# Kernel tuning notes

Measured on AMD Instinct MI355X. Metric: run time of the kernel, lower is better.

The kernel has to match this reference:

```python
import jax, jax.numpy as jnp
import numpy as np
from jax import lax

D_MODEL = 1024
D_INNER = 2 * D_MODEL  # expand=2
D_CONV = 4
BATCH = 4
SEQ = 4096


def setup_inputs() -> dict:
    key = jax.random.key(0)
    ks = jax.random.split(key, 10)
    s = 0.02
    return {
        "x": jax.random.normal(ks[0], (BATCH, SEQ, D_MODEL), jnp.float32),
        "in_proj_w": jax.random.normal(ks[1], (2 * D_INNER, D_MODEL), jnp.float32) * s,
        "in_proj_b": jnp.zeros((2 * D_INNER,), jnp.float32),
        "conv_w": jax.random.normal(ks[2], (D_INNER, 1, D_CONV), jnp.float32) * s,
        "conv_b": jnp.zeros((D_INNER,), jnp.float32),
        "dt_w": jax.random.normal(ks[3], (D_INNER, D_INNER), jnp.float32) * s,
        "dt_b": jnp.zeros((D_INNER,), jnp.float32),
        "b_w": jax.random.normal(ks[4], (D_INNER, D_INNER), jnp.float32) * s,
        "c_w": jax.random.normal(ks[5], (D_INNER, D_INNER), jnp.float32) * s,
        "A_log": jax.random.normal(ks[6], (D_INNER,), jnp.float32) * 0.02 - 2.0,
        "D_param": jnp.ones((D_INNER,), jnp.float32),
        "out_w": jax.random.normal(ks[7], (D_MODEL, D_INNER), jnp.float32) * s,
        "out_b": jnp.zeros((D_MODEL,), jnp.float32),
    }


def _mixer(x, in_proj_w, in_proj_b, conv_w, conv_b, dt_w, dt_b,
           b_w, c_w, A_log, D_param, out_w, out_b):
    B, L, _ = x.shape
    # input projection -> split into x/z branches
    xz = jnp.einsum("bld,ed->ble", x, in_proj_w) + in_proj_b
    x_branch, z_branch = jnp.split(xz, 2, axis=-1)  # each [B, L, d_inner]

    # causal depthwise conv1d (padding=d_conv-1 on the left == torch pad then [:L])
    u = jnp.transpose(x_branch, (0, 2, 1))  # [B, d_inner, L]
    u = lax.conv_general_dilated(
        u, conv_w,
        window_strides=(1,),
        padding=[(D_CONV - 1, 0)],
        dimension_numbers=("NCH", "OIH", "NCH"),
        feature_group_count=D_INNER,
    ) + conv_b[None, :, None]
    u = jnp.transpose(u, (0, 2, 1))  # [B, L, d_inner]
    u = jax.nn.silu(u)

    dt = jax.nn.softplus(jnp.einsum("bld,ed->ble", u, dt_w) + dt_b) + 1e-4
    B_t = jnp.tanh(jnp.einsum("bld,ed->ble", u, b_w))
    C_t = jnp.tanh(jnp.einsum("bld,ed->ble", u, c_w))

    A = jnp.exp(A_log)  # [d_inner]
    decay = jnp.exp(-dt * A)          # [B, L, d_inner]
    inc = (1.0 - decay) * B_t * u     # [B, L, d_inner]

    # linear recurrence: state_t = decay_t * state_{t-1} + inc_t
    def step(state, xs):
        d_t, i_t = xs
        state = d_t * state + i_t
        return state, state

    init = jnp.zeros((B, D_INNER), x.dtype)
    _, states = lax.scan(step, init,
                         (jnp.transpose(decay, (1, 0, 2)),
                          jnp.transpose(inc, (1, 0, 2))))  # [L, B, d_inner]
    states = jnp.transpose(states, (1, 0, 2))  # [B, L, d_inner]

    y = C_t * states + D_param * u
    y = y * jax.nn.sigmoid(z_branch)  # SiLU-style gate
    # dropout is identity in eval mode
    return jnp.einsum("ble,de->bld", y, out_w) + out_b


def reference(x, in_proj_w, in_proj_b, conv_w, conv_b, dt_w, dt_b,
              b_w, c_w, A_log, D_param, out_w, out_b):
    return _mixer(x, in_proj_w, in_proj_b, conv_w, conv_b, dt_w, dt_b,
                  b_w, c_w, A_log, D_param, out_w, out_b)
```

## Files before the change

### kernel.cpp

```cpp
#include <hip/hip_runtime.h>
#include <math.h>
#include <stdint.h>


#define BATCH 4
#define SEQ 4096
#define DMODEL 1024
#define DINNER 2048
#define CLS 32

typedef __bf16 bf16_t;
typedef __bf16 bf16x8 __attribute__((ext_vector_type(8)));
typedef float f32x4 __attribute__((ext_vector_type(4)));
typedef unsigned short ushort_t;
typedef unsigned short u16x4 __attribute__((ext_vector_type(4)));

enum { EP_F32 = 0, EP_BF = 1, EP_DBC = 2, EP_GATE = 3 };

__device__ __forceinline__ void gload_lds16(const void* g, void* l) {
    __builtin_amdgcn_global_load_lds(
        (const __attribute__((address_space(1))) void*)g,
        (__attribute__((address_space(3))) void*)l, 16, 0, 0);
}

__device__ __forceinline__ ushort_t f2bf(float f) {
    union { float f; uint32_t u; } c; c.f = f;
    uint32_t u = c.u;
    u += 0x7fffu + ((u >> 16) & 1u);
    return (ushort_t)(u >> 16);
}
__device__ __forceinline__ float bf2f(ushort_t h) {
    union { uint32_t u; float f; } c; c.u = (uint32_t)h << 16;
    return c.f;
}
__device__ __forceinline__ float tanh_exact(float v) {
    v = fminf(fmaxf(v, -15.f), 15.f);
    float e = __expf(2.f * v);
    return (e - 1.f) / (e + 1.f);
}
__device__ __forceinline__ float tanh_poly(float v) {
    float v2 = v * v;
    float t = v * (1.f - v2 * (0.33333333f - 0.13333333f * v2));
    if (__builtin_expect(fabsf(v) > 0.25f, 0)) t = tanh_exact(v);
    return t;
}
__device__ __forceinline__ float softplus_poly(float v) {
    float v2 = v * v;
    float s = 0.69314718f + 0.5f * v + v2 * (0.125f - 0.0052083333f * v2);
    if (__builtin_expect(fabsf(v) > 0.25f, 0))
        s = fmaxf(v, 0.f) + __logf(1.f + __expf(-fabsf(v)));
    return s;
}

#define WAITV2 asm volatile("s_waitcnt vmcnt(2)" ::: "memory")
#define WAITV0 asm volatile("s_waitcnt vmcnt(0)" ::: "memory")
#define WAITL0 asm volatile("s_waitcnt lgkmcnt(0)" ::: "memory")

__global__ __launch_bounds__(512) void gemm256_ep(
    const bf16_t* __restrict__ A, const bf16_t* __restrict__ W,
    const float* __restrict__ bias,
    ushort_t* __restrict__ T0, ushort_t* __restrict__ T1,
    ushort_t* __restrict__ T2, const float* __restrict__ alogp,
    int K, int Nout, int Lc, int a_bstride, int a_l0,
    int c_bstride, int c_l0, int mode)
{
    __shared__ __align__(16) char smem[131072];
    const int tid = threadIdx.x;
    const int lane = tid & 63;
    const int wid = tid >> 6;
    const int wm2 = wid >> 2;
    const int wn2 = wid & 3;
    const int wz = blockIdx.z;
    const bf16_t* Wmat = W + (size_t)wz * Nout * K;
    ushort_t* Tz = (wz == 0) ? T0 : (wz == 1 ? T1 : T2);
    const int n0 = blockIdx.x * 256;
    const int m0 = blockIdx.y * 256;
    const int bb = m0 / Lc;
    const int lb = m0 - bb * Lc;
    const bf16_t* Abase = A + ((size_t)bb * a_bstride + a_l0 + lb) * K;
    const bf16_t* Wbase = Wmat + (size_t)n0 * K;

    int r_[2], c_[2], lofs_[2];
#pragma unroll
    for (int i = 0; i < 2; ++i) {
        int ofs = tid * 16 + i * 8192;
        int r = ofs >> 7;
        int c16 = (ofs >> 4) & 7;
        r_[i] = r;
        c_[i] = (c16 ^ (r & 7)) << 3;
        lofs_[i] = ofs;
    }

    const int nt = K / 64;

    f32x4 acc[4][4][2];
#pragma unroll
    for (int q = 0; q < 4; ++q)
#pragma unroll
        for (int mi = 0; mi < 4; ++mi)
#pragma unroll
            for (int ni = 0; ni < 2; ++ni) acc[q][mi][ni] = f32x4{0.f, 0.f, 0.f, 0.f};

#pragma unroll
    for (int s = 0; s < 4; ++s) {
        const int isB_ = (s == 1 || s == 2);
        const int h_ = (s >= 2) ? 1 : 0;
        char* dst_ = smem + (isB_ ? 32768 : 0) + h_ * 16384;
        const bf16_t* g_ = isB_ ? Wbase : Abase;
        gload_lds16(g_ + (size_t)(h_ * 128 + r_[0]) * K + c_[0], dst_ + lofs_[0]);
        gload_lds16(g_ + (size_t)(h_ * 128 + r_[1]) * K + c_[1], dst_ + lofs_[1]);
    }

#define STAGE(S)                                                              \
    if (t + 1 < nt) {                                                         \
      char* base_ = smem + (((t + 1) & 1) ? 65536 : 0);                       \
      const int isB_ = ((S) == 1 || (S) == 2);                                \
      const int h_ = ((S) >= 2) ? 1 : 0;                                      \
      char* dst_ = base_ + (isB_ ? 32768 : 0) + h_ * 16384;                   \
      const bf16_t* g_ = isB_ ? Wbase : Abase;                                \
      const int k0_ = (t + 1) * 64;                                           \
      gload_lds16(g_ + (size_t)(h_ * 128 + r_[0]) * K + k0_ + c_[0],          \
                  dst_ + lofs_[0]);                                           \
      gload_lds16(g_ + (size_t)(h_ * 128 + r_[1]) * K + k0_ + c_[1],          \
                  dst_ + lofs_[1]);                                           \
    }

#define READ_A(dst, half)                                                     \
    _Pragma("unroll") for (int mi = 0; mi < 4; ++mi)                          \
    _Pragma("unroll") for (int ks = 0; ks < 2; ++ks) {                        \
      int row = (half) * 128 + wm2 * 64 + mi * 16 + (lane & 15);              \
      int cb = (ks * 64 + ((lane >> 4) << 4)) ^ ((row & 7) << 4);             \
      dst[mi][ks] = *(const bf16x8*)(bufb + row * 128 + cb);                  \
    }

#define READ_B(dst, half)                                                     \
    _Pragma("unroll") for (int ni = 0; ni < 2; ++ni)                          \
    _Pragma("unroll") for (int ks = 0; ks < 2; ++ks) {                        \
      int row = (half) * 128 + wn2 * 32 + ni * 16 + (lane & 15);              \
      int cb = (ks * 64 + ((lane >> 4) << 4)) ^ ((row & 7) << 4);             \
      dst[ni][ks] = *(const bf16x8*)(bufb + 32768 + row * 128 + cb);          \
    }

#define MMA(Q, AV, BV)                                                        \
    __builtin_amdgcn_s_setprio(1);                                            \
    _Pragma("unroll") for (int ks = 0; ks < 2; ++ks)                          \
    _Pragma("unroll") for (int mi = 0; mi < 4; ++mi)                          \
    _Pragma("unroll") for (int ni = 0; ni < 2; ++ni)                          \
      acc[(Q)][mi][ni] = __builtin_amdgcn_mfma_f32_16x16x32_bf16(             \
          AV[mi][ks], BV[ni][ks], acc[(Q)][mi][ni], 0, 0, 0);                 \
    __builtin_amdgcn_s_setprio(0);

    for (int t = 0; t < nt; ++t) {
        const char* bufb = smem + ((t & 1) ? 65536 : 0);
        bf16x8 av0[4][2], av1[4][2], bv0[2][2], bv1[2][2];
        STAGE(0)
        if (t + 1 < nt) { WAITV2; } else { WAITV0; }
        __builtin_amdgcn_s_barrier();
        READ_A(av0, 0)
        READ_B(bv0, 0)
        WAITL0; __builtin_amdgcn_sched_barrier(0);
        MMA(0, av0, bv0)
        STAGE(1)
        READ_B(bv1, 1)
        WAITL0; __builtin_amdgcn_sched_barrier(0);
        MMA(1, av0, bv1)
        STAGE(2)
        READ_A(av1, 1)
        WAITL0; __builtin_amdgcn_sched_barrier(0);
        MMA(3, av1, bv1)
        STAGE(3)
        MMA(2, av1, bv0)
        __builtin_amdgcn_s_barrier();
    }
#undef STAGE
#undef READ_A
#undef READ_B
#undef MMA

    __syncthreads();

    const size_t rowbase = (size_t)bb * c_bstride + c_l0 + lb;
    ushort_t* sm = (ushort_t*)smem;
#pragma unroll
    for (int q = 0; q < 4; ++q) {
#pragma unroll
        for (int ni = 0; ni < 2; ++ni) {
            const int col = (q & 1) * 128 + wn2 * 32 + ni * 16 + (lane & 15);
            float bv = 0.f, Ae = 0.f;
            if (mode == EP_BF || mode == EP_GATE) bv = bias[n0 + col];
            else if (mode == EP_DBC && wz == 0) {
                bv = bias[n0 + col]; Ae = __expf(alogp[n0 + col]);
            }
#pragma unroll
            for (int mi = 0; mi < 4; ++mi) {
#pragma unroll
                for (int r4 = 0; r4 < 4; ++r4) {
                    const int row = (q >> 1) * 128 + wm2 * 64 + mi * 16 +
                                    ((lane >> 4) << 2) + r4;
                    float v = acc[q][mi][ni][r4] + bv;
                    ushort_t o;
                    if (mode == EP_BF) {
                        o = f2bf(v);
                    } else if (mode == EP_GATE) {
                        const size_t off = (rowbase + row) * (size_t)Nout + n0 + col;
                        o = f2bf(bf2f(Tz[off]) / (1.f + __expf(-v)));
                    } else {
                        if (wz == 0)
                            o = f2bf(__expf(-(softplus_poly(v) + 1e-4f) * Ae));
                        else
                            o = f2bf(tanh_poly(v));
                    }
                    const int sbyte = row * 512 + (((col * 2) ^ ((row & 7) << 4)));
                    *(ushort_t*)((char*)sm + sbyte) = o;
                }
            }
        }
    }
    __syncthreads();
#pragma unroll
    for (int it = 0; it < 16; ++it) {
        const int b0 = tid * 16 + it * 8192;
        const int row = b0 >> 9;
        const int inrow = b0 & 511;
        const int src = row * 512 + (inrow ^ ((row & 7) << 4));
        int4 vv = *(const int4*)((const char*)sm + src);
        *(int4*)(Tz + (rowbase + row) * (size_t)Nout + n0 + (inrow >> 1)) = vv;
    }
}

#define GBK 64

__global__ __launch_bounds__(256) void gemm_f32out(
    const bf16_t* __restrict__ A, const bf16_t* __restrict__ W,
    const float* __restrict__ bias, float* __restrict__ Cf,
    int K, int Nout, int Lc, int a_bstride, int a_l0,
    int c_bstride, int c_l0)
{
    __shared__ __align__(16) bf16_t smem[128 * 128];
    bf16_t* sA = smem;
    bf16_t* sB = smem + 128 * GBK;
    const int tid = threadIdx.x;
    const int lane = tid & 63;
    const int wid = tid >> 6;
    const int wm = wid >> 1, wn = wid & 1;
    const int n0 = blockIdx.x * 128;
    const int m0 = blockIdx.y * 128;
    const int bb = m0 / Lc;
    const int lb = m0 - bb * Lc;
    const bf16_t* Abase = A + ((size_t)bb * a_bstride + a_l0 + lb) * K;
    const bf16_t* Wbase = W + (size_t)n0 * K;

    int st_row[4], st_sc[4], st_ofs[4];
#pragma unroll
    for (int i = 0; i < 4; ++i) {
        int ofs = tid * 16 + i * 4096;
        int r = ofs >> 7;
        int c16 = (ofs >> 4) & 7;
        st_ofs[i] = ofs;
        st_row[i] = r;
        st_sc[i] = (c16 ^ (r & 7)) << 3;
    }

    f32x4 acc[4][4];
#pragma unroll
    for (int i = 0; i < 4; ++i)
#pragma unroll
        for (int j = 0; j < 4; ++j) acc[i][j] = f32x4{0.f, 0.f, 0.f, 0.f};

    for (int k0 = 0; k0 < K; k0 += GBK) {
#pragma unroll
        for (int i = 0; i < 4; ++i) {
            gload_lds16(Abase + (size_t)st_row[i] * K + k0 + st_sc[i],
                        (char*)sA + st_ofs[i]);
            gload_lds16(Wbase + (size_t)st_row[i] * K + k0 + st_sc[i],
                        (char*)sB + st_ofs[i]);
        }
        __syncthreads();
#pragma unroll
        for (int ks = 0; ks < 2; ++ks) {
            bf16x8 av[4], bv[4];
#pragma unroll
            for (int mi = 0; mi < 4; ++mi) {
                int row = wm * 64 + mi * 16 + (lane & 15);
                int cb = (ks * 64 + ((lane >> 4) << 4)) ^ ((row & 7) << 4);
                av[mi] = *(const bf16x8*)((const char*)sA + row * 128 + cb);
            }
#pragma unroll
            for (int ni = 0; ni < 4; ++ni) {
                int row = wn * 64 + ni * 16 + (lane & 15);
                int cb = (ks * 64 + ((lane >> 4) << 4)) ^ ((row & 7) << 4);
                bv[ni] = *(const bf16x8*)((const char*)sB + row * 128 + cb);
            }
#pragma unroll
            for (int mi = 0; mi < 4; ++mi)
#pragma unroll
                for (int ni = 0; ni < 4; ++ni)
                    acc[mi][ni] = __builtin_amdgcn_mfma_f32_16x16x32_bf16(
                        av[mi], bv[ni], acc[mi][ni], 0, 0, 0);
        }
        __syncthreads();
    }

    const size_t rowbase = (size_t)bb * c_bstride + c_l0 + lb;
#pragma unroll
    for (int ni = 0; ni < 4; ++ni) {
        const int coll = wn * 64 + ni * 16 + (lane & 15);
        const float bv = bias ? bias[n0 + coll] : 0.f;
#pragma unroll
        for (int mi = 0; mi < 4; ++mi) {
#pragma unroll
            for (int r4 = 0; r4 < 4; ++r4) {
                const int rowl = wm * 64 + mi * 16 + ((lane >> 4) << 2) + r4;
                Cf[(rowbase + rowl) * (size_t)Nout + n0 + coll] =
                    acc[mi][ni][r4] + bv;
            }
        }
    }
}

__global__ __launch_bounds__(256) void cvt_bf16_k(
    const float4* __restrict__ in, ushort4* __restrict__ out, int n4)
{
    for (int i = blockIdx.x * 256 + threadIdx.x; i < n4; i += gridDim.x * 256) {
        float4 v = in[i];
        ushort4 o;
        o.x = f2bf(v.x); o.y = f2bf(v.y); o.z = f2bf(v.z); o.w = f2bf(v.w);
        out[i] = o;
    }
}

__global__ __launch_bounds__(256) void conv_silu_bf(
    const ushort_t* __restrict__ xb, const ushort_t* __restrict__ tailb,
    const float* __restrict__ cw, const float* __restrict__ cb,
    ushort_t* __restrict__ ubf, int Lc, int l0, size_t total)
{
    for (size_t idx = (size_t)blockIdx.x * 256 + threadIdx.x; idx < total;
         idx += (size_t)gridDim.x * 256) {
        int e = (int)(idx % DINNER);
        size_t r = idx / DINNER;
        int lp = (int)(r % Lc);
        int b  = (int)(r / Lc);
        float4 w = *(const float4*)(cw + (size_t)e * 4);
        float s = cb[e];
        const ushort_t* xbase = xb + (size_t)b * Lc * DINNER + e;
        if (lp >= 3) {
            s += bf2f(xbase[(size_t)(lp - 3) * DINNER]) * w.x
               + bf2f(xbase[(size_t)(lp - 2) * DINNER]) * w.y
               + bf2f(xbase[(size_t)(lp - 1) * DINNER]) * w.z
               + bf2f(xbase[(size_t)lp * DINNER]) * w.w;
        } else {
            const float ws4[4] = {w.x, w.y, w.z, w.w};
            const ushort_t* tbase = tailb + (size_t)b * 3 * DINNER + e;
#pragma unroll
            for (int j = 0; j < 4; ++j) {
                int ls = lp - 3 + j;
                float v;
                if (ls >= 0)            v = bf2f(xbase[(size_t)ls * DINNER]);
                else if (l0 + ls >= 0)  v = bf2f(tbase[(size_t)(3 + ls) * DINNER]);
                else                    v = 0.f;
                s += v * ws4[j];
            }
        }
        ubf[idx] = f2bf(s / (1.f + __expf(-s)));
    }
}

__global__ __launch_bounds__(256) void tail_update_bf(
    const ushort_t* __restrict__ xb, ushort_t* __restrict__ tailb, int Lc)
{
    int idx = blockIdx.x * 256 + threadIdx.x;
    if (idx >= BATCH * 3 * DINNER) return;
    int e = idx % DINNER;
    int j = (idx / DINNER) % 3;
    int b = idx / (3 * DINNER);
    tailb[idx] = xb[((size_t)b * Lc + Lc - 3 + j) * DINNER + e];
}

__global__ __launch_bounds__(256) void scan1_v4(
    const ushort_t* __restrict__ dec, const ushort_t* __restrict__ bt,
    const ushort_t* __restrict__ ub,
    float* __restrict__ P, float* __restrict__ S, int Lc, int nsub)
{
    int t = blockIdx.x * 256 + threadIdx.x;
    int e = (t & 511) << 2;
    int rest = t >> 9;
    int c = rest % nsub;
    int b = rest / nsub;
    size_t off = ((size_t)b * Lc + (size_t)c * CLS) * DINNER + e;
    float p[4] = {1.f, 1.f, 1.f, 1.f};
    float s[4] = {0.f, 0.f, 0.f, 0.f};
    for (int t0 = 0; t0 < CLS; ++t0) {
        size_t o = off + (size_t)t0 * DINNER;
        u16x4 d4 = *(const u16x4*)(dec + o);
        u16x4 b4 = *(const u16x4*)(bt + o);
        u16x4 u4 = *(const u16x4*)(ub + o);
#pragma unroll
        for (int j = 0; j < 4; ++j) {
            float d = bf2f(d4[j]);
            float inc = (1.f - d) * bf2f(b4[j]) * bf2f(u4[j]);
            s[j] = d * s[j] + inc;
            p[j] *= d;
        }
    }
    size_t po = ((size_t)b * nsub + c) * DINNER + e;
    *(float4*)(P + po) = float4{p[0], p[1], p[2], p[3]};
    *(float4*)(S + po) = float4{s[0], s[1], s[2], s[3]};
}

__global__ __launch_bounds__(256) void scan_p2(
    float* __restrict__ P, float* __restrict__ S,
    float* __restrict__ carry, int nsub, int first)
{
    int idx = blockIdx.x * 256 + threadIdx.x;
    int e = idx % DINNER;
    int b = idx / DINNER;
    float cv = first ? 0.f : carry[idx];
    for (int c = 0; c < nsub; ++c) {
        size_t o = ((size_t)b * nsub + c) * DINNER + e;
        float p = P[o], s = S[o];
        P[o] = cv;
        cv = p * cv + s;
    }
    carry[idx] = cv;
}

__global__ __launch_bounds__(256) void p3y_v4(
    const ushort_t* __restrict__ dec, ushort_t* __restrict__ bty,
    const ushort_t* __restrict__ ct, const ushort_t* __restrict__ ub,
    const float* __restrict__ Dp, const float* __restrict__ Pc,
    int Lc, int nsub)
{
    int t = blockIdx.x * 256 + threadIdx.x;
    int e = (t & 511) << 2;
    int rest = t >> 9;
    int c = rest % nsub;
    int b = rest / nsub;
    size_t off = ((size_t)b * Lc + (size_t)c * CLS) * DINNER + e;
    size_t po = ((size_t)b * nsub + c) * DINNER + e;
    float4 stv = *(const float4*)(Pc + po);
    float4 Dv  = *(const float4*)(Dp + e);
    float st[4] = {stv.x, stv.y, stv.z, stv.w};
    float D4[4] = {Dv.x, Dv.y, Dv.z, Dv.w};
    for (int t0 = 0; t0 < CLS; ++t0) {
        size_t o = off + (size_t)t0 * DINNER;
        u16x4 d4 = *(const u16x4*)(dec + o);
        u16x4 b4 = *(const u16x4*)(bty + o);
        u16x4 c4 = *(const u16x4*)(ct + o);
        u16x4 u4 = *(const u16x4*)(ub + o);
        u16x4 y4;
#pragma unroll
        for (int j = 0; j < 4; ++j) {
            float d = bf2f(d4[j]);
            float u = bf2f(u4[j]);
            float inc = (1.f - d) * bf2f(b4[j]) * u;
            st[j] = d * st[j] + inc;
            y4[j] = f2bf(bf2f(c4[j]) * st[j] + D4[j] * u);
        }
        *(u16x4*)(bty + o) = y4;
    }
}

extern "C" void kernel_launch(void* const* d_in, const int* in_sizes, int n_in,
                              void* d_out, int out_size, void* d_ws, size_t ws_size,
                              hipStream_t stream)
{
    const float* x    = (const float*)d_in[0];
    const float* ipw  = (const float*)d_in[1];
    const float* ipb  = (const float*)d_in[2];
    const float* cw   = (const float*)d_in[3];
    const float* cb   = (const float*)d_in[4];
    const float* dtw  = (const float*)d_in[5];
    const float* dtb  = (const float*)d_in[6];
    const float* bw   = (const float*)d_in[7];
    const float* cwt  = (const float*)d_in[8];
    const float* alog = (const float*)d_in[9];
    const float* dpar = (const float*)d_in[10];
    const float* ow   = (const float*)d_in[11];
    const float* ob   = (const float*)d_in[12];
    float* out = (float*)d_out;

    const size_t XN   = (size_t)BATCH * SEQ * DMODEL;
    const size_t WIP  = (size_t)2 * DINNER * DMODEL;
    const size_t WSQ  = (size_t)DINNER * DINNER;
    const size_t WOUT = (size_t)DMODEL * DINNER;
    const size_t const_bytes = 2 * (XN + WIP + 3 * WSQ + WOUT);

    const int cands[5] = {4096, 2048, 1024, 512, 256};
    int Lc = 256;
    for (int i = 0; i < 5; ++i) {
        size_t NBe = (size_t)BATCH * cands[i] * DINNER;
        size_t need = const_bytes
                    + 4 * NBe * 2
                    + (size_t)BATCH * 3 * DINNER * 2
                    + (size_t)BATCH * DINNER * 4
                    + 2 * (size_t)BATCH * (cands[i] / CLS) * DINNER * 4
                    + 1024;
        if (need <= ws_size) { Lc = cands[i]; break; }
    }
    const int nsub = Lc / CLS;
    const size_t NBe = (size_t)BATCH * Lc * DINNER;

    char* p = (char*)d_ws;
    ushort_t* xbf   = (ushort_t*)p; p += XN * 2;
    ushort_t* ipwbf = (ushort_t*)p; p += WIP * 2;
    ushort_t* wcat  = (ushort_t*)p; p += 3 * WSQ * 2;
    ushort_t* owbf  = (ushort_t*)p; p += WOUT * 2;
    ushort_t* S1 = (ushort_t*)p; p += NBe * 2;
    ushort_t* S2 = (ushort_t*)p; p += NBe * 2;
    ushort_t* S3 = (ushort_t*)p; p += NBe * 2;
    ushort_t* S4 = (ushort_t*)p; p += NBe * 2;
    ushort_t* tailb = (ushort_t*)p; p += (size_t)BATCH * 3 * DINNER * 2;
    float* carry = (float*)p; p += (size_t)BATCH * DINNER * 4;
    float* Pb    = (float*)p; p += (size_t)BATCH * nsub * DINNER * 4;
    float* Sb    = (float*)p;

    const dim3 blk(256);
    const dim3 blk512(512);
    const int M = BATCH * Lc;
    const dim3 g256(DINNER / 256, M / 256, 1);
    const dim3 g256z3(DINNER / 256, M / 256, 3);
    const dim3 gOut(DMODEL / 128, M / 128, 1);
    const int pwBlocks = (int)(((NBe + 255) / 256 < 4096) ? (NBe + 255) / 256 : 4096);
    const int scanBlocks = BATCH * nsub * 2;

    auto cvt = [&](const float* in, ushort_t* outp, size_t n) {
        int n4 = (int)(n / 4);
        int g = n4 / 256 < 2048 ? (n4 + 255) / 256 : 2048;
        cvt_bf16_k<<<g, blk, 0, stream>>>((const float4*)in, (ushort4*)outp, n4);
    };
    cvt(x, xbf, XN);
    cvt(ipw, ipwbf, WIP);
    cvt(dtw, wcat, WSQ);
    cvt(bw, wcat + WSQ, WSQ);
    cvt(cwt, wcat + 2 * WSQ, WSQ);
    cvt(ow, owbf, WOUT);

    const int nchunks = SEQ / Lc;
    for (int c = 0; c < nchunks; ++c) {
        const int l0 = c * Lc;
        gemm256_ep<<<g256, blk512, 0, stream>>>(
            (const bf16_t*)xbf, (const bf16_t*)ipwbf, ipb,
            S1, nullptr, nullptr, nullptr,
            DMODEL, DINNER, Lc, SEQ, l0, Lc, 0, EP_BF);
        conv_silu_bf<<<pwBlocks, blk, 0, stream>>>(S1, tailb, cw, cb, S2, Lc, l0, NBe);
        if (nchunks > 1)
            tail_update_bf<<<BATCH * 3 * DINNER / 256, blk, 0, stream>>>(S1, tailb, Lc);
        gemm256_ep<<<g256z3, blk512, 0, stream>>>(
            (const bf16_t*)S2, (const bf16_t*)wcat, dtb,
            S3, S4, S1, alog,
            DINNER, DINNER, Lc, Lc, 0, Lc, 0, EP_DBC);
        scan1_v4<<<scanBlocks, blk, 0, stream>>>(S3, S4, S2, Pb, Sb, Lc, nsub);
        scan_p2<<<BATCH * DINNER / 256, blk, 0, stream>>>(Pb, Sb, carry, nsub, c == 0);
        p3y_v4<<<scanBlocks, blk, 0, stream>>>(S3, S4, S1, S2, dpar, Pb, Lc, nsub);
        gemm256_ep<<<g256, blk512, 0, stream>>>(
            (const bf16_t*)xbf, (const bf16_t*)(ipwbf + (size_t)DINNER * DMODEL),
            ipb + DINNER, S4, nullptr, nullptr, nullptr,
            DMODEL, DINNER, Lc, SEQ, l0, Lc, 0, EP_GATE);
        gemm_f32out<<<gOut, blk, 0, stream>>>(
            (const bf16_t*)S4, (const bf16_t*)owbf, ob,
            out, DINNER, DMODEL, Lc, Lc, 0, SEQ, l0);
    }
}
```

Baseline: 984.4 us.

## Route output projection through 256-tile pipelined GEMM and batch LDS reads

Replaces the simple 128x128 output-projection GEMM with the pipelined 256x256 gemm256_ep kernel, using a new fp32-store epilogue mode. It also removes the explicit lgkmcnt waits and sched barriers inside the main loop and issues all four LDS fragment reads up front. This lets the compiler schedule the waits and gives the output GEMM better data reuse and pipelining. The trade-offs are fewer blocks for the output GEMM (M/256 x 4), higher register pressure from holding all fragments at once, and uncoalesced direct fp32 stores.

```diff
diff --git a/kernel.cpp b/kernel.cpp
--- a/kernel.cpp
+++ b/kernel.cpp
@@ -54,11 +54,10 @@
 
 #define WAITV2 asm volatile("s_waitcnt vmcnt(2)" ::: "memory")
 #define WAITV0 asm volatile("s_waitcnt vmcnt(0)" ::: "memory")
-#define WAITL0 asm volatile("s_waitcnt lgkmcnt(0)" ::: "memory")
 
 __global__ __launch_bounds__(512) void gemm256_ep(
     const bf16_t* __restrict__ A, const bf16_t* __restrict__ W,
-    const float* __restrict__ bias,
+    const float* __restrict__ bias, float* __restrict__ Cf,
     ushort_t* __restrict__ T0, ushort_t* __restrict__ T1,
     ushort_t* __restrict__ T2, const float* __restrict__ alogp,
     int K, int Nout, int Lc, int a_bstride, int a_l0,
@@ -158,15 +157,12 @@
         __builtin_amdgcn_s_barrier();
         READ_A(av0, 0)
         READ_B(bv0, 0)
-        WAITL0; __builtin_amdgcn_sched_barrier(0);
+        READ_B(bv1, 1)
+        READ_A(av1, 1)
         MMA(0, av0, bv0)
         STAGE(1)
-        READ_B(bv1, 1)
-        WAITL0; __builtin_amdgcn_sched_barrier(0);
         MMA(1, av0, bv1)
         STAGE(2)
-        READ_A(av1, 1)
-        WAITL0; __builtin_amdgcn_sched_barrier(0);
         MMA(3, av1, bv1)
         STAGE(3)
         MMA(2, av1, bv0)
@@ -180,6 +176,28 @@
     __syncthreads();
 
     const size_t rowbase = (size_t)bb * c_bstride + c_l0 + lb;
+    if (mode == EP_F32) {
+#pragma unroll
+        for (int q = 0; q < 4; ++q) {
+#pragma unroll
+            for (int ni = 0; ni < 2; ++ni) {
+                const int col = (q & 1) * 128 + wn2 * 32 + ni * 16 + (lane & 15);
+                const float bv = bias ? bias[n0 + col] : 0.f;
+#pragma unroll
+                for (int mi = 0; mi < 4; ++mi) {
+#pragma unroll
+                    for (int r4 = 0; r4 < 4; ++r4) {
+                        const int row = (q >> 1) * 128 + wm2 * 64 + mi * 16 +
+                                        ((lane >> 4) << 2) + r4;
+                        Cf[(rowbase + row) * (size_t)Nout + n0 + col] =
+                            acc[q][mi][ni][r4] + bv;
+                    }
+                }
+            }
+        }
+        return;
+    }
+
     ushort_t* sm = (ushort_t*)smem;
 #pragma unroll
     for (int q = 0; q < 4; ++q) {
@@ -228,96 +246,6 @@
     }
 }
 
-#define GBK 64
-
-__global__ __launch_bounds__(256) void gemm_f32out(
-    const bf16_t* __restrict__ A, const bf16_t* __restrict__ W,
-    const float* __restrict__ bias, float* __restrict__ Cf,
-    int K, int Nout, int Lc, int a_bstride, int a_l0,
-    int c_bstride, int c_l0)
-{
-    __shared__ __align__(16) bf16_t smem[128 * 128];
-    bf16_t* sA = smem;
-    bf16_t* sB = smem + 128 * GBK;
-    const int tid = threadIdx.x;
-    const int lane = tid & 63;
-    const int wid = tid >> 6;
-    const int wm = wid >> 1, wn = wid & 1;
-    const int n0 = blockIdx.x * 128;
-    const int m0 = blockIdx.y * 128;
-    const int bb = m0 / Lc;
-    const int lb = m0 - bb * Lc;
-    const bf16_t* Abase = A + ((size_t)bb * a_bstride + a_l0 + lb) * K;
-    const bf16_t* Wbase = W + (size_t)n0 * K;
-
-    int st_row[4], st_sc[4], st_ofs[4];
-#pragma unroll
-    for (int i = 0; i < 4; ++i) {
-        int ofs = tid * 16 + i * 4096;
-        int r = ofs >> 7;
-        int c16 = (ofs >> 4) & 7;
-        st_ofs[i] = ofs;
-        st_row[i] = r;
-        st_sc[i] = (c16 ^ (r & 7)) << 3;
-    }
-
-    f32x4 acc[4][4];
-#pragma unroll
-    for (int i = 0; i < 4; ++i)
-#pragma unroll
-        for (int j = 0; j < 4; ++j) acc[i][j] = f32x4{0.f, 0.f, 0.f, 0.f};
-
-    for (int k0 = 0; k0 < K; k0 += GBK) {
-#pragma unroll
-        for (int i = 0; i < 4; ++i) {
-            gload_lds16(Abase + (size_t)st_row[i] * K + k0 + st_sc[i],
-                        (char*)sA + st_ofs[i]);
-            gload_lds16(Wbase + (size_t)st_row[i] * K + k0 + st_sc[i],
-                        (char*)sB + st_ofs[i]);
-        }
-        __syncthreads();
-#pragma unroll
-        for (int ks = 0; ks < 2; ++ks) {
-            bf16x8 av[4], bv[4];
-#pragma unroll
-            for (int mi = 0; mi < 4; ++mi) {
-                int row = wm * 64 + mi * 16 + (lane & 15);
-                int cb = (ks * 64 + ((lane >> 4) << 4)) ^ ((row & 7) << 4);
-                av[mi] = *(const bf16x8*)((const char*)sA + row * 128 + cb);
-            }
-#pragma unroll
-            for (int ni = 0; ni < 4; ++ni) {
-                int row = wn * 64 + ni * 16 + (lane & 15);
-                int cb = (ks * 64 + ((lane >> 4) << 4)) ^ ((row & 7) << 4);
-                bv[ni] = *(const bf16x8*)((const char*)sB + row * 128 + cb);
-            }
-#pragma unroll
-            for (int mi = 0; mi < 4; ++mi)
-#pragma unroll
-                for (int ni = 0; ni < 4; ++ni)
-                    acc[mi][ni] = __builtin_amdgcn_mfma_f32_16x16x32_bf16(
-                        av[mi], bv[ni], acc[mi][ni], 0, 0, 0);
-        }
-        __syncthreads();
-    }
-
-    const size_t rowbase = (size_t)bb * c_bstride + c_l0 + lb;
-#pragma unroll
-    for (int ni = 0; ni < 4; ++ni) {
-        const int coll = wn * 64 + ni * 16 + (lane & 15);
-        const float bv = bias ? bias[n0 + coll] : 0.f;
-#pragma unroll
-        for (int mi = 0; mi < 4; ++mi) {
-#pragma unroll
-            for (int r4 = 0; r4 < 4; ++r4) {
-                const int rowl = wm * 64 + mi * 16 + ((lane >> 4) << 2) + r4;
-                Cf[(rowbase + rowl) * (size_t)Nout + n0 + coll] =
-                    acc[mi][ni][r4] + bv;
-            }
-        }
-    }
-}
-
 __global__ __launch_bounds__(256) void cvt_bf16_k(
     const float4* __restrict__ in, ushort4* __restrict__ out, int n4)
 {
@@ -519,7 +447,7 @@
     const int M = BATCH * Lc;
     const dim3 g256(DINNER / 256, M / 256, 1);
     const dim3 g256z3(DINNER / 256, M / 256, 3);
-    const dim3 gOut(DMODEL / 128, M / 128, 1);
+    const dim3 g256out(DMODEL / 256, M / 256, 1);
     const int pwBlocks = (int)(((NBe + 255) / 256 < 4096) ? (NBe + 255) / 256 : 4096);
     const int scanBlocks = BATCH * nsub * 2;
 
@@ -540,24 +468,25 @@
         const int l0 = c * Lc;
         gemm256_ep<<<g256, blk512, 0, stream>>>(
             (const bf16_t*)xbf, (const bf16_t*)ipwbf, ipb,
-            S1, nullptr, nullptr, nullptr,
+            nullptr, S1, nullptr, nullptr, nullptr,
             DMODEL, DINNER, Lc, SEQ, l0, Lc, 0, EP_BF);
         conv_silu_bf<<<pwBlocks, blk, 0, stream>>>(S1, tailb, cw, cb, S2, Lc, l0, NBe);
         if (nchunks > 1)
             tail_update_bf<<<BATCH * 3 * DINNER / 256, blk, 0, stream>>>(S1, tailb, Lc);
         gemm256_ep<<<g256z3, blk512, 0, stream>>>(
             (const bf16_t*)S2, (const bf16_t*)wcat, dtb,
-            S3, S4, S1, alog,
+            nullptr, S3, S4, S1, alog,
             DINNER, DINNER, Lc, Lc, 0, Lc, 0, EP_DBC);
         scan1_v4<<<scanBlocks, blk, 0, stream>>>(S3, S4, S2, Pb, Sb, Lc, nsub);
         scan_p2<<<BATCH * DINNER / 256, blk, 0, stream>>>(Pb, Sb, carry, nsub, c == 0);
         p3y_v4<<<scanBlocks, blk, 0, stream>>>(S3, S4, S1, S2, dpar, Pb, Lc, nsub);
         gemm256_ep<<<g256, blk512, 0, stream>>>(
             (const bf16_t*)xbf, (const bf16_t*)(ipwbf + (size_t)DINNER * DMODEL),
-            ipb + DINNER, S4, nullptr, nullptr, nullptr,
+            ipb + DINNER, nullptr, S4, nullptr, nullptr, nullptr,
             DMODEL, DINNER, Lc, SEQ, l0, Lc, 0, EP_GATE);
-        gemm_f32out<<<gOut, blk, 0, stream>>>(
+        gemm256_ep<<<g256out, blk512, 0, stream>>>(
             (const bf16_t*)S4, (const bf16_t*)owbf, ob,
-            out, DINNER, DMODEL, Lc, Lc, 0, SEQ, l0);
-    }
-}
+            out, nullptr, nullptr, nullptr, nullptr,
+            DINNER, DMODEL, Lc, Lc, 0, SEQ, l0, EP_F32);
+    }
+}
```

New measurement: 1.025 ms. 1.04x slower.
